# Optimization experiments

Measured on AMD Instinct MI355X. Metric: run time of the kernel, lower is better.

The kernel has to match this reference:

```python
import jax, jax.numpy as jnp
import numpy as np

ALPHA = 0.2  # LeakyReLU negative slope used by GAT attention


def _seg_softmax(scores, rows, n):
    # numerically stable softmax of per-edge scores grouped by destination row
    m = jax.ops.segment_max(scores, rows, num_segments=n)
    ex = jnp.exp(scores - m[rows])
    s = jax.ops.segment_sum(ex, rows, num_segments=n)
    return ex / s[rows]


def setup_inputs() -> dict:
    key = jax.random.key(0)
    ks = jax.random.split(key, 10)
    VOCAB, U, N, DEG = 200000, 50000, 20000, 16
    DIN, DOUT, H, ETYPES, EDIM = 64, 64, 4, 32, 64
    node_features = jax.random.normal(ks[0], (VOCAB, DIN), jnp.float32)
    W = jax.random.normal(ks[1], (H, DIN, DOUT), jnp.float32) * np.float32(np.sqrt(2.0 / (DIN + DOUT)))
    a_pos = jax.random.normal(ks[2], (H, 2 * DOUT), jnp.float32) * 0.1
    a_neg = jax.random.normal(ks[3], (H, 2 * DOUT), jnp.float32) * 0.1
    edge_embedding = jax.random.normal(ks[4], (ETYPES, EDIM), jnp.float32)
    edge_transform = jax.random.normal(ks[5], (EDIM, DOUT), jnp.float32) * np.float32(np.sqrt(2.0 / (EDIM + DOUT)))
    unique_nodes = jax.random.randint(ks[6], (U,), 0, VOCAB)
    row_unique = jax.random.randint(ks[7], (N,), 0, U)  # index of each output row's own node in the unique list
    # pos adjacency with self edges appended (adj_pos2 in the source)
    pos_row = jnp.concatenate([jnp.repeat(jnp.arange(N), DEG), jnp.arange(N)])
    pos_col = jnp.concatenate([jax.random.randint(ks[8], (N * DEG,), 0, U), row_unique])
    neg_row = jnp.repeat(jnp.arange(N), DEG)
    neg_col = jax.random.randint(ks[9], (N * DEG,), 0, U)
    return {
        "node_features": node_features, "W": W, "a_pos": a_pos, "a_neg": a_neg,
        "edge_embedding": edge_embedding, "edge_transform": edge_transform,
        "unique_nodes": unique_nodes, "row_unique": row_unique,
        "pos_row": pos_row, "pos_col": pos_col, "neg_row": neg_row, "neg_col": neg_col,
        "n_rows": N,
    }


def reference(node_features, W, a_pos, a_neg, edge_embedding, edge_transform,
              unique_nodes, row_unique, pos_row, pos_col, neg_row, neg_col, n_rows):
    embed = node_features[unique_nodes]                 # [U, Din] gather of unique node embeddings
    Wh = jnp.einsum('ud,hdo->huo', embed, W)            # [H, U, Dout]
    Dout = W.shape[-1]
    rows_all = jnp.concatenate([pos_row, neg_row])
    cols_all = jnp.concatenate([pos_col, neg_col])

    def head(Wh_h, ap, an):
        # per-node score halves (GAT trick: a^T[h_i || h_j] = a_dst.h_i + a_src.h_j)
        dst_p = (Wh_h @ ap[:Dout])[row_unique]          # [N]
        src_p = Wh_h @ ap[Dout:]                        # [U]
        dst_n = (Wh_h @ an[:Dout])[row_unique]
        src_n = Wh_h @ an[Dout:]
        e_pos = jax.nn.leaky_relu(dst_p[pos_row] + src_p[pos_col], ALPHA)
        e_neg = jax.nn.leaky_relu(dst_n[neg_row] + src_n[neg_col], ALPHA)
        att = _seg_softmax(jnp.concatenate([e_pos, e_neg]), rows_all, n_rows)  # joint softmax over pos+neg edges
        return jax.ops.segment_sum(att[:, None] * Wh_h[cols_all], rows_all, num_segments=n_rows)

    outs = jax.vmap(head)(Wh, a_pos, a_neg)             # [H, N, Dout]
    h_hidden = jax.nn.relu(jnp.transpose(outs, (1, 0, 2)).reshape(outs.shape[1], -1))  # concat heads -> ReLU
    edge_out = edge_embedding @ edge_transform          # edge-type projection
    return (h_hidden, edge_out)
```

## Files before the change

### kernel.cpp

```cpp
#include <hip/hip_runtime.h>
#include <hip/hip_bf16.h>
#include <hip/hip_fp16.h>
#include <math.h>

#define LRELU_ALPHA 0.2f

typedef __attribute__((ext_vector_type(8))) short bf16x8;
typedef __attribute__((ext_vector_type(4))) float f32x4;

__device__ __forceinline__ unsigned short f2bf(float f) {
    union { float f; unsigned u; } v; v.f = f;
    unsigned r = v.u + 0x7fffu + ((v.u >> 16) & 1u);
    return (unsigned short)(r >> 16);
}
__device__ __forceinline__ unsigned cvtpk(float lo, float hi) {
    unsigned r;
    asm("v_cvt_pk_bf16_f32 %0, %1, %2" : "=v"(r) : "v"(lo), "v"(hi));
    return r;
}
__device__ __forceinline__ __half2 u2h2(unsigned u) {
    union { unsigned u; __half2 h; } x; x.u = u; return x.h;
}
__device__ __forceinline__ unsigned h22u(__half2 h) {
    union { __half2 h; unsigned u; } x; x.h = h; return x.u;
}

__global__ void prep_kernel(const float* __restrict__ W,
                            const float* __restrict__ a_pos, const float* __restrict__ a_neg,
                            const float* __restrict__ ee, const float* __restrict__ et,
                            unsigned short* __restrict__ Wt, unsigned short* __restrict__ avB,
                            float* __restrict__ edge_out, int H, int ET) {
    const int HE = H * 4096, AV = H * 256;
    int t = blockIdx.x * blockDim.x + threadIdx.x;
    if (t < HE) {
        int k = t & 63, n = (t >> 6) & 63, h = t >> 12;
        Wt[((size_t)h * 64 + n) * 64 + k] = f2bf(W[(size_t)h * 4096 + k * 64 + n]);
    } else if (t < HE + AV) {
        int s = t - HE;
        int k = s & 63, q = (s >> 6) & 3, h = s >> 8;
        const float* a  = (q < 2 ? a_pos : a_neg) + (size_t)h * 128 + (q & 1) * 64;
        const float* wr = W + (size_t)h * 4096 + k * 64;
        float v = 0.f;
#pragma unroll
        for (int o = 0; o < 64; o += 4) {
            const float4 wv = *(const float4*)(wr + o);
            const float4 av = *(const float4*)(a + o);
            v = fmaf(wv.x, av.x, fmaf(wv.y, av.y, fmaf(wv.z, av.z, fmaf(wv.w, av.w, v))));
        }
        avB[((size_t)h * 4 + q) * 64 + k] = f2bf(v);
    } else {
        int s = t - HE - AV;
        if (s < ET * 64) {
            int e = s >> 6, o = s & 63;
            float acc = 0.f;
#pragma unroll
            for (int k = 0; k < 64; ++k)
                acc = fmaf(ee[e * 64 + k], et[k * 64 + o], acc);
            edge_out[s] = acc;
        }
    }
}

__global__ __launch_bounds__(256) void score_cvt_kernel(
    const float* __restrict__ nf, const unsigned short* __restrict__ avB,
    const int* __restrict__ un, unsigned short* __restrict__ embed16,
    float2* __restrict__ sc_dst, float2* __restrict__ sc_src, int U)
{
    const int wave = threadIdx.x >> 6;
    const int lane = threadIdx.x & 63;
    const int grp  = lane >> 4;
    const int r    = lane & 15;
    const long u0  = (long)blockIdx.x * 64 + wave * 16;
    if (u0 >= U) return;
    const long u  = u0 + r;
    const long ur = (u < U) ? u : (long)(U - 1);

    const float* erow = nf + (size_t)un[ur] * 64 + grp * 8;
    const float4 e0 = *(const float4*)(erow);
    const float4 e1 = *(const float4*)(erow + 4);
    const float4 e2 = *(const float4*)(erow + 32);
    const float4 e3 = *(const float4*)(erow + 36);

    union { unsigned d[4]; bf16x8 v; } A0, A1;
    A0.d[0] = cvtpk(e0.x, e0.y); A0.d[1] = cvtpk(e0.z, e0.w);
    A0.d[2] = cvtpk(e1.x, e1.y); A0.d[3] = cvtpk(e1.z, e1.w);
    A1.d[0] = cvtpk(e2.x, e2.y); A1.d[1] = cvtpk(e2.z, e2.w);
    A1.d[2] = cvtpk(e3.x, e3.y); A1.d[3] = cvtpk(e3.z, e3.w);

    if (u < U) {
        union { __half2 h2[4]; uint4 v; } F0, F1;
        F0.h2[0] = __floats2half2_rn(e0.x, e0.y); F0.h2[1] = __floats2half2_rn(e0.z, e0.w);
        F0.h2[2] = __floats2half2_rn(e1.x, e1.y); F0.h2[3] = __floats2half2_rn(e1.z, e1.w);
        F1.h2[0] = __floats2half2_rn(e2.x, e2.y); F1.h2[1] = __floats2half2_rn(e2.z, e2.w);
        F1.h2[2] = __floats2half2_rn(e3.x, e3.y); F1.h2[3] = __floats2half2_rn(e3.z, e3.w);
        *(uint4*)(embed16 + (size_t)u * 64 + grp * 8)      = F0.v;
        *(uint4*)(embed16 + (size_t)u * 64 + 32 + grp * 8) = F1.v;
    }

    f32x4 acc = (f32x4)(0.f);
    const unsigned short* wp = avB + (size_t)r * 64 + grp * 8;
    bf16x8 b0 = *(const bf16x8*)wp;
    bf16x8 b1 = *(const bf16x8*)(wp + 32);
    acc = __builtin_amdgcn_mfma_f32_16x16x32_bf16(b0, A0.v, acc, 0, 0, 0);
    acc = __builtin_amdgcn_mfma_f32_16x16x32_bf16(b1, A1.v, acc, 0, 0, 0);

    if (u < U) {
        sc_dst[(size_t)u * 4 + grp] = make_float2(acc[0], acc[2]);
        sc_src[(size_t)u * 4 + grp] = make_float2(acc[1], acc[3]);
    }
}

__global__ __launch_bounds__(256) void agg4_kernel(
    const int* __restrict__ pos_col, const int* __restrict__ neg_col,
    const unsigned short* __restrict__ embed16,
    const float2* __restrict__ sc_dst, const float2* __restrict__ sc_src,
    unsigned short* __restrict__ aggb, int N, int U)
{
    constexpr int DP = 16, NE = 33, NEP = 34;
    __shared__ int  s_col[4][NEP];
    __shared__ uint4 s_att[4][NEP];

    const int wave = threadIdx.x >> 6;
    const int lane = threadIdx.x & 63;
    const int i = blockIdx.x * 4 + wave;
    if (i >= N) return;

    int col = 0;
    if (lane < DP)       col = pos_col[(size_t)i * DP + lane];
    else if (lane == DP) col = pos_col[(size_t)N * DP + i];
    else if (lane < NE)  col = neg_col[(size_t)i * 16 + (lane - DP - 1)];

    const float4* ssv = (const float4*)sc_src;
    const float4 sA = ssv[2 * (size_t)(unsigned)col];
    const float4 sB = ssv[2 * (size_t)(unsigned)col + 1];
    const int u0s = __shfl(col, DP, 64);
    const float4* sdv = (const float4*)sc_dst;
    const float4 dA = sdv[2 * (size_t)(unsigned)u0s];
    const float4 dB = sdv[2 * (size_t)(unsigned)u0s + 1];

    const bool isp = (lane <= DP);
    float s0 = isp ? dA.x + sA.x : dA.y + sA.y;
    float s1 = isp ? dA.z + sA.z : dA.w + sA.w;
    float s2 = isp ? dB.x + sB.x : dB.y + sB.y;
    float s3 = isp ? dB.z + sB.z : dB.w + sB.w;
    s0 = (s0 > 0.f) ? s0 : LRELU_ALPHA * s0;
    s1 = (s1 > 0.f) ? s1 : LRELU_ALPHA * s1;
    s2 = (s2 > 0.f) ? s2 : LRELU_ALPHA * s2;
    s3 = (s3 > 0.f) ? s3 : LRELU_ALPHA * s3;
    if (lane >= NE) { s0 = s1 = s2 = s3 = -INFINITY; }

    float m0 = s0, m1 = s1, m2 = s2, m3 = s3;
#pragma unroll
    for (int off = 32; off; off >>= 1) {
        m0 = fmaxf(m0, __shfl_xor(m0, off, 64));
        m1 = fmaxf(m1, __shfl_xor(m1, off, 64));
        m2 = fmaxf(m2, __shfl_xor(m2, off, 64));
        m3 = fmaxf(m3, __shfl_xor(m3, off, 64));
    }
    const float x0 = (lane < NE) ? __expf(s0 - m0) : 0.f;
    const float x1 = (lane < NE) ? __expf(s1 - m1) : 0.f;
    const float x2 = (lane < NE) ? __expf(s2 - m2) : 0.f;
    const float x3 = (lane < NE) ? __expf(s3 - m3) : 0.f;
    float S0 = x0, S1 = x1, S2 = x2, S3 = x3;
#pragma unroll
    for (int off = 32; off; off >>= 1) {
        S0 += __shfl_xor(S0, off, 64);
        S1 += __shfl_xor(S1, off, 64);
        S2 += __shfl_xor(S2, off, 64);
        S3 += __shfl_xor(S3, off, 64);
    }
    const float a0f = __fdividef(x0, S0), a1f = __fdividef(x1, S1);
    const float a2f = __fdividef(x2, S2), a3f = __fdividef(x3, S3);

    if (lane < NEP) {
        uint4 a4;
        a4.x = h22u(__float2half2_rn(a0f));
        a4.y = h22u(__float2half2_rn(a1f));
        a4.z = h22u(__float2half2_rn(a2f));
        a4.w = h22u(__float2half2_rn(a3f));
        s_col[wave][lane] = col;
        s_att[wave][lane] = a4;
    }

    const int half = lane >> 5, mlo = lane & 31;
    const char* eb = (const char*)embed16 + (mlo << 2);
    __half2 ac0 = __float2half2_rn(0.f), ac1 = ac0, ac2 = ac0, ac3 = ac0;
#pragma unroll
    for (int t = 0; t < 17; ++t) {
        const int e = 2 * t + half;
        const int ce = s_col[wave][e];
        const uint4 a4 = s_att[wave][e];
        const unsigned v = *(const unsigned*)(eb + ((size_t)(unsigned)ce << 7));
        const __half2 vh = u2h2(v);
        ac0 = __hfma2(u2h2(a4.x), vh, ac0);
        ac1 = __hfma2(u2h2(a4.y), vh, ac1);
        ac2 = __hfma2(u2h2(a4.z), vh, ac2);
        ac3 = __hfma2(u2h2(a4.w), vh, ac3);
    }
    float2 f0 = __half22float2(ac0), f1 = __half22float2(ac1);
    float2 f2 = __half22float2(ac2), f3 = __half22float2(ac3);
    f0.x += __shfl_xor(f0.x, 32, 64); f0.y += __shfl_xor(f0.y, 32, 64);
    f1.x += __shfl_xor(f1.x, 32, 64); f1.y += __shfl_xor(f1.y, 32, 64);
    f2.x += __shfl_xor(f2.x, 32, 64); f2.y += __shfl_xor(f2.y, 32, 64);
    f3.x += __shfl_xor(f3.x, 32, 64); f3.y += __shfl_xor(f3.y, 32, 64);
    if (lane < 32) {
        unsigned* ap = (unsigned*)(aggb + (size_t)i * 256);
        ap[0 * 32 + mlo] = cvtpk(f0.x, f0.y);
        ap[1 * 32 + mlo] = cvtpk(f1.x, f1.y);
        ap[2 * 32 + mlo] = cvtpk(f2.x, f2.y);
        ap[3 * 32 + mlo] = cvtpk(f3.x, f3.y);
    }
}

__global__ __launch_bounds__(256) void out_gemm_kernel(
    const unsigned short* __restrict__ aggb, const unsigned short* __restrict__ Wt,
    float* __restrict__ out, int N, int H)
{
    const int wave = threadIdx.x >> 6;
    const int lane = threadIdx.x & 63;
    const int grp  = lane >> 4;
    const int r    = lane & 15;
    const long j = (long)blockIdx.x * 4 + wave;
    const int  h = (int)(j % H);
    const long i0 = (j / H) * 16;
    if (i0 >= N) return;
    const long i  = i0 + r;
    const long ir = (i < N) ? i : (long)(N - 1);

    const unsigned short* arow = aggb + ((size_t)ir * H + h) * 64 + grp * 8;
    bf16x8 a0 = *(const bf16x8*)arow;
    bf16x8 a1 = *(const bf16x8*)(arow + 32);

    f32x4 acc[4];
#pragma unroll
    for (int nt = 0; nt < 4; ++nt) {
        acc[nt] = (f32x4)(0.f);
        const unsigned short* wp = Wt + (((size_t)h * 64 + nt * 16 + r) * 64 + grp * 8);
        bf16x8 b0 = *(const bf16x8*)wp;
        bf16x8 b1 = *(const bf16x8*)(wp + 32);
        acc[nt] = __builtin_amdgcn_mfma_f32_16x16x32_bf16(b0, a0, acc[nt], 0, 0, 0);
        acc[nt] = __builtin_amdgcn_mfma_f32_16x16x32_bf16(b1, a1, acc[nt], 0, 0, 0);
    }
    if (i < N) {
        float* orow = out + ((size_t)i * H + h) * 64;
#pragma unroll
        for (int nt = 0; nt < 4; ++nt) {
            float4 o;
            o.x = fmaxf(acc[nt][0], 0.f); o.y = fmaxf(acc[nt][1], 0.f);
            o.z = fmaxf(acc[nt][2], 0.f); o.w = fmaxf(acc[nt][3], 0.f);
            *(float4*)(orow + nt * 16 + grp * 4) = o;
        }
    }
}

__global__ void embed_cvt_generic(const float* __restrict__ nf, const int* __restrict__ un,
                                  unsigned short* __restrict__ embed16, int U) {
    long t = (long)blockIdx.x * blockDim.x + threadIdx.x;
    if (t >= (long)U * 64) return;
    union { __half h; unsigned short s; } c;
    c.h = __float2half_rn(nf[(size_t)un[t >> 6] * 64 + (t & 63)]);
    embed16[t] = c.s;
}
__global__ void score_generic(const unsigned short* __restrict__ embed16,
                              const unsigned short* __restrict__ avB,
                              float2* __restrict__ sc_dst, float2* __restrict__ sc_src,
                              int U, int H) {
    long t = (long)blockIdx.x * blockDim.x + threadIdx.x;
    if (t >= (long)U * H) return;
    const long u = t / H; const int h = (int)(t % H);
    float s[4];
    for (int q = 0; q < 4; ++q) {
        float acc = 0.f;
        for (int k = 0; k < 64; ++k) {
            union { unsigned short s; __half h; } w; w.s = embed16[u * 64 + k];
            union { unsigned u; float f; } b; b.u = ((unsigned)avB[((size_t)h * 4 + q) * 64 + k]) << 16;
            acc = fmaf(__half2float(w.h), b.f, acc);
        }
        s[q] = acc;
    }
    sc_dst[u * H + h] = make_float2(s[0], s[2]);
    sc_src[u * H + h] = make_float2(s[1], s[3]);
}
__global__ __launch_bounds__(256) void agg_generic(
    const int* __restrict__ pos_col, const int* __restrict__ neg_col,
    const unsigned short* __restrict__ embed16,
    const float2* __restrict__ sc_dst, const float2* __restrict__ sc_src,
    unsigned short* __restrict__ aggb, int N, int U, int DEGP, int DEGN, int H)
{
    const int wave = threadIdx.x >> 6;
    const int lane = threadIdx.x & 63;
    const long j = (long)blockIdx.x * 4 + wave;
    const int i = (int)(j % N);
    const int h = (int)(j / N);
    if (h >= H) return;
    const int NE = DEGP + 1 + DEGN;

    int col = 0;
    if (lane < DEGP)       col = pos_col[(size_t)i * DEGP + lane];
    else if (lane == DEGP) col = pos_col[(size_t)N * DEGP + i];
    else if (lane < NE)    col = neg_col[(size_t)i * DEGN + (lane - DEGP - 1)];
    const float2 ss = sc_src[(size_t)col * H + h];
    const int u0s = __shfl(col, DEGP, 64);
    const float2 sd = sc_dst[(size_t)u0s * H + h];
    float score = -INFINITY;
    if (lane < NE) {
        const float raw = (lane <= DEGP) ? sd.x + ss.x : sd.y + ss.y;
        score = (raw > 0.f) ? raw : LRELU_ALPHA * raw;
    }
    float m = score;
#pragma unroll
    for (int off = 32; off; off >>= 1) m = fmaxf(m, __shfl_xor(m, off, 64));
    const float ex = (lane < NE) ? __expf(score - m) : 0.f;
    float S = ex;
#pragma unroll
    for (int off = 32; off; off >>= 1) S += __shfl_xor(S, off, 64);
    const float att = __fdividef(ex, S);

    float acc = 0.f;
    for (int e = 0; e < NE; ++e) {
        const int   ce = __shfl(col, e, 64);
        const float ae = __shfl(att, e, 64);
        union { unsigned short s; __half h; } w; w.s = embed16[(size_t)(unsigned)ce * 64 + lane];
        acc = fmaf(ae, __half2float(w.h), acc);
    }
    aggb[((size_t)i * H + h) * 64 + lane] = f2bf(acc);
}

extern "C" void kernel_launch(void* const* d_in, const int* in_sizes, int n_in,
                              void* d_out, int out_size, void* d_ws, size_t ws_size,
                              hipStream_t stream) {
    const float* nf     = (const float*)d_in[0];
    const float* W      = (const float*)d_in[1];
    const float* a_pos  = (const float*)d_in[2];
    const float* a_neg  = (const float*)d_in[3];
    const float* ee     = (const float*)d_in[4];
    const float* et     = (const float*)d_in[5];
    const int* unique_nodes = (const int*)d_in[6];
    const int* pos_col  = (const int*)d_in[9];
    const int* neg_col  = (const int*)d_in[11];

    const int U    = in_sizes[6];
    const int N    = in_sizes[7];
    const int Epos = in_sizes[8];
    const int Eneg = in_sizes[10];
    const int H    = in_sizes[1] / (64 * 64);
    const int DEGN = Eneg / N;
    const int DEGP = Epos / N - 1;
    const int ET   = in_sizes[4] / 64;

    char* ws = (char*)d_ws;
    auto alloc = [&](size_t bytes) { char* p = ws; ws += (bytes + 255) & ~(size_t)255; return p; };
    unsigned short* embed16 = (unsigned short*)alloc((size_t)U * 64 * 2);
    float2*         sc_dst  = (float2*)alloc((size_t)U * H * 8);
    float2*         sc_src  = (float2*)alloc((size_t)U * H * 8);
    unsigned short* aggb    = (unsigned short*)alloc((size_t)N * H * 64 * 2);
    unsigned short* Wt      = (unsigned short*)alloc((size_t)H * 4096 * 2);
    unsigned short* avB     = (unsigned short*)alloc((size_t)H * 256 * 2);
    float* out = (float*)d_out;

    const int PT = H * 4096 + H * 256 + ET * 64;
    prep_kernel<<<(PT + 255) / 256, 256, 0, stream>>>(W, a_pos, a_neg, ee, et, Wt, avB,
                                                      out + (size_t)N * H * 64, H, ET);

    if (H == 4 && DEGP == 16 && DEGN == 16) {
        score_cvt_kernel<<<(U + 63) / 64, 256, 0, stream>>>(nf, avB, unique_nodes,
                                                            embed16, sc_dst, sc_src, U);
        agg4_kernel<<<(N + 3) / 4, 256, 0, stream>>>(pos_col, neg_col, embed16,
                                                     sc_dst, sc_src, aggb, N, U);
    } else {
        embed_cvt_generic<<<(int)(((long)U * 64 + 255) / 256), 256, 0, stream>>>(
            nf, unique_nodes, embed16, U);
        score_generic<<<(int)(((long)U * H + 255) / 256), 256, 0, stream>>>(
            embed16, avB, sc_dst, sc_src, U, H);
        agg_generic<<<(int)(((long)N * H + 3) / 4), 256, 0, stream>>>(
            pos_col, neg_col, embed16, sc_dst, sc_src, aggb, N, U, DEGP, DEGN, H);
    }

    const long tiles = ((long)N + 15) / 16;
    out_gemm_kernel<<<(int)((tiles * H + 3) / 4), 256, 0, stream>>>(aggb, Wt, out, N, H);
}
```

Baseline: 49.48 us.

## Fuse attention aggregation with per-head output GEMM and drop softmax max pass

Merges the aggregation kernel and the output projection GEMM into one 512-thread kernel. Each wave aggregates two destination rows, the 16 rows per block are staged in LDS as fp16, and four waves then run fp16 MFMA against W to write the ReLU output directly. This removes the global round trip of the intermediate aggregate buffer and one kernel launch. It also switches W and the MFMA path from bf16 to fp16, and drops the max-subtraction reduction in the softmax, which risks exp overflow for large scores. A new N%16 requirement gates the fast path.

```diff
diff --git a/kernel.cpp b/kernel.cpp
--- a/kernel.cpp
+++ b/kernel.cpp
@@ -7,11 +7,15 @@
 
 typedef __attribute__((ext_vector_type(8))) short bf16x8;
 typedef __attribute__((ext_vector_type(4))) float f32x4;
+typedef _Float16 f16x8 __attribute__((ext_vector_type(8)));
 
 __device__ __forceinline__ unsigned short f2bf(float f) {
     union { float f; unsigned u; } v; v.f = f;
     unsigned r = v.u + 0x7fffu + ((v.u >> 16) & 1u);
     return (unsigned short)(r >> 16);
+}
+__device__ __forceinline__ unsigned short f2h(float f) {
+    union { __half h; unsigned short s; } c; c.h = __float2half_rn(f); return c.s;
 }
 __device__ __forceinline__ unsigned cvtpk(float lo, float hi) {
     unsigned r;
@@ -34,7 +38,7 @@
     int t = blockIdx.x * blockDim.x + threadIdx.x;
     if (t < HE) {
         int k = t & 63, n = (t >> 6) & 63, h = t >> 12;
-        Wt[((size_t)h * 64 + n) * 64 + k] = f2bf(W[(size_t)h * 4096 + k * 64 + n]);
+        Wt[((size_t)h * 64 + n) * 64 + k] = f2h(W[(size_t)h * 4096 + k * 64 + n]);
     } else if (t < HE + AV) {
         int s = t - HE;
         int k = s & 63, q = (s >> 6) & 3, h = s >> 8;
@@ -110,139 +114,169 @@
     }
 }
 
-__global__ __launch_bounds__(256) void agg4_kernel(
+__global__ __launch_bounds__(512) void aggemm_kernel(
     const int* __restrict__ pos_col, const int* __restrict__ neg_col,
     const unsigned short* __restrict__ embed16,
     const float2* __restrict__ sc_dst, const float2* __restrict__ sc_src,
-    unsigned short* __restrict__ aggb, int N, int U)
+    const unsigned short* __restrict__ Wt,
+    float* __restrict__ out, int N, int U)
 {
-    constexpr int DP = 16, NE = 33, NEP = 34;
-    __shared__ int  s_col[4][NEP];
-    __shared__ uint4 s_att[4][NEP];
+    constexpr int DP = 16, NE = 33, NEP = 36;
+    __shared__ int   s_col[8][2][NEP];
+    __shared__ uint4 s_att[8][2][NEP];
+    __shared__ __align__(16) unsigned short s_agg[16][256];
 
     const int wave = threadIdx.x >> 6;
     const int lane = threadIdx.x & 63;
-    const int i = blockIdx.x * 4 + wave;
-    if (i >= N) return;
-
-    int col = 0;
-    if (lane < DP)       col = pos_col[(size_t)i * DP + lane];
-    else if (lane == DP) col = pos_col[(size_t)N * DP + i];
-    else if (lane < NE)  col = neg_col[(size_t)i * 16 + (lane - DP - 1)];
+    const int iA = blockIdx.x * 16 + wave * 2;
+    const int iB = iA + 1;
+
+    int colA = 0, colB = 0;
+    if (lane < DP)       { colA = pos_col[(size_t)iA * DP + lane];
+                           colB = pos_col[(size_t)iB * DP + lane]; }
+    else if (lane == DP) { colA = pos_col[(size_t)N * DP + iA];
+                           colB = pos_col[(size_t)N * DP + iB]; }
+    else if (lane < NE)  { colA = neg_col[(size_t)iA * 16 + (lane - DP - 1)];
+                           colB = neg_col[(size_t)iB * 16 + (lane - DP - 1)]; }
 
     const float4* ssv = (const float4*)sc_src;
-    const float4 sA = ssv[2 * (size_t)(unsigned)col];
-    const float4 sB = ssv[2 * (size_t)(unsigned)col + 1];
-    const int u0s = __shfl(col, DP, 64);
+    const float4 sA0 = ssv[2 * (size_t)(unsigned)colA];
+    const float4 sA1 = ssv[2 * (size_t)(unsigned)colA + 1];
+    const float4 sB0 = ssv[2 * (size_t)(unsigned)colB];
+    const float4 sB1 = ssv[2 * (size_t)(unsigned)colB + 1];
+    const int uA = __shfl(colA, DP, 64), uB = __shfl(colB, DP, 64);
     const float4* sdv = (const float4*)sc_dst;
-    const float4 dA = sdv[2 * (size_t)(unsigned)u0s];
-    const float4 dB = sdv[2 * (size_t)(unsigned)u0s + 1];
+    const float4 dA0 = sdv[2 * (size_t)(unsigned)uA];
+    const float4 dA1 = sdv[2 * (size_t)(unsigned)uA + 1];
+    const float4 dB0 = sdv[2 * (size_t)(unsigned)uB];
+    const float4 dB1 = sdv[2 * (size_t)(unsigned)uB + 1];
 
     const bool isp = (lane <= DP);
-    float s0 = isp ? dA.x + sA.x : dA.y + sA.y;
-    float s1 = isp ? dA.z + sA.z : dA.w + sA.w;
-    float s2 = isp ? dB.x + sB.x : dB.y + sB.y;
-    float s3 = isp ? dB.z + sB.z : dB.w + sB.w;
-    s0 = (s0 > 0.f) ? s0 : LRELU_ALPHA * s0;
-    s1 = (s1 > 0.f) ? s1 : LRELU_ALPHA * s1;
-    s2 = (s2 > 0.f) ? s2 : LRELU_ALPHA * s2;
-    s3 = (s3 > 0.f) ? s3 : LRELU_ALPHA * s3;
-    if (lane >= NE) { s0 = s1 = s2 = s3 = -INFINITY; }
-
-    float m0 = s0, m1 = s1, m2 = s2, m3 = s3;
+    float a_s0 = isp ? dA0.x + sA0.x : dA0.y + sA0.y;
+    float a_s1 = isp ? dA0.z + sA0.z : dA0.w + sA0.w;
+    float a_s2 = isp ? dA1.x + sA1.x : dA1.y + sA1.y;
+    float a_s3 = isp ? dA1.z + sA1.z : dA1.w + sA1.w;
+    float b_s0 = isp ? dB0.x + sB0.x : dB0.y + sB0.y;
+    float b_s1 = isp ? dB0.z + sB0.z : dB0.w + sB0.w;
+    float b_s2 = isp ? dB1.x + sB1.x : dB1.y + sB1.y;
+    float b_s3 = isp ? dB1.z + sB1.z : dB1.w + sB1.w;
+    a_s0 = (a_s0 > 0.f) ? a_s0 : LRELU_ALPHA * a_s0;
+    a_s1 = (a_s1 > 0.f) ? a_s1 : LRELU_ALPHA * a_s1;
+    a_s2 = (a_s2 > 0.f) ? a_s2 : LRELU_ALPHA * a_s2;
+    a_s3 = (a_s3 > 0.f) ? a_s3 : LRELU_ALPHA * a_s3;
+    b_s0 = (b_s0 > 0.f) ? b_s0 : LRELU_ALPHA * b_s0;
+    b_s1 = (b_s1 > 0.f) ? b_s1 : LRELU_ALPHA * b_s1;
+    b_s2 = (b_s2 > 0.f) ? b_s2 : LRELU_ALPHA * b_s2;
+    b_s3 = (b_s3 > 0.f) ? b_s3 : LRELU_ALPHA * b_s3;
+
+    const bool act = (lane < NE);
+    float ax0 = act ? __expf(a_s0) : 0.f, ax1 = act ? __expf(a_s1) : 0.f;
+    float ax2 = act ? __expf(a_s2) : 0.f, ax3 = act ? __expf(a_s3) : 0.f;
+    float bx0 = act ? __expf(b_s0) : 0.f, bx1 = act ? __expf(b_s1) : 0.f;
+    float bx2 = act ? __expf(b_s2) : 0.f, bx3 = act ? __expf(b_s3) : 0.f;
+    float aS0 = ax0, aS1 = ax1, aS2 = ax2, aS3 = ax3;
+    float bS0 = bx0, bS1 = bx1, bS2 = bx2, bS3 = bx3;
 #pragma unroll
     for (int off = 32; off; off >>= 1) {
-        m0 = fmaxf(m0, __shfl_xor(m0, off, 64));
-        m1 = fmaxf(m1, __shfl_xor(m1, off, 64));
-        m2 = fmaxf(m2, __shfl_xor(m2, off, 64));
-        m3 = fmaxf(m3, __shfl_xor(m3, off, 64));
-    }
-    const float x0 = (lane < NE) ? __expf(s0 - m0) : 0.f;
-    const float x1 = (lane < NE) ? __expf(s1 - m1) : 0.f;
-    const float x2 = (lane < NE) ? __expf(s2 - m2) : 0.f;
-    const float x3 = (lane < NE) ? __expf(s3 - m3) : 0.f;
-    float S0 = x0, S1 = x1, S2 = x2, S3 = x3;
-#pragma unroll
-    for (int off = 32; off; off >>= 1) {
-        S0 += __shfl_xor(S0, off, 64);
-        S1 += __shfl_xor(S1, off, 64);
-        S2 += __shfl_xor(S2, off, 64);
-        S3 += __shfl_xor(S3, off, 64);
-    }
-    const float a0f = __fdividef(x0, S0), a1f = __fdividef(x1, S1);
-    const float a2f = __fdividef(x2, S2), a3f = __fdividef(x3, S3);
-
+        aS0 += __shfl_xor(aS0, off, 64); aS1 += __shfl_xor(aS1, off, 64);
+        aS2 += __shfl_xor(aS2, off, 64); aS3 += __shfl_xor(aS3, off, 64);
+        bS0 += __shfl_xor(bS0, off, 64); bS1 += __shfl_xor(bS1, off, 64);
+        bS2 += __shfl_xor(bS2, off, 64); bS3 += __shfl_xor(bS3, off, 64);
+    }
     if (lane < NEP) {
-        uint4 a4;
-        a4.x = h22u(__float2half2_rn(a0f));
-        a4.y = h22u(__float2half2_rn(a1f));
-        a4.z = h22u(__float2half2_rn(a2f));
-        a4.w = h22u(__float2half2_rn(a3f));
-        s_col[wave][lane] = col;
-        s_att[wave][lane] = a4;
-    }
-
-    const int half = lane >> 5, mlo = lane & 31;
-    const char* eb = (const char*)embed16 + (mlo << 2);
-    __half2 ac0 = __float2half2_rn(0.f), ac1 = ac0, ac2 = ac0, ac3 = ac0;
-#pragma unroll
-    for (int t = 0; t < 17; ++t) {
-        const int e = 2 * t + half;
-        const int ce = s_col[wave][e];
-        const uint4 a4 = s_att[wave][e];
-        const unsigned v = *(const unsigned*)(eb + ((size_t)(unsigned)ce << 7));
-        const __half2 vh = u2h2(v);
-        ac0 = __hfma2(u2h2(a4.x), vh, ac0);
-        ac1 = __hfma2(u2h2(a4.y), vh, ac1);
-        ac2 = __hfma2(u2h2(a4.z), vh, ac2);
-        ac3 = __hfma2(u2h2(a4.w), vh, ac3);
-    }
-    float2 f0 = __half22float2(ac0), f1 = __half22float2(ac1);
-    float2 f2 = __half22float2(ac2), f3 = __half22float2(ac3);
-    f0.x += __shfl_xor(f0.x, 32, 64); f0.y += __shfl_xor(f0.y, 32, 64);
-    f1.x += __shfl_xor(f1.x, 32, 64); f1.y += __shfl_xor(f1.y, 32, 64);
-    f2.x += __shfl_xor(f2.x, 32, 64); f2.y += __shfl_xor(f2.y, 32, 64);
-    f3.x += __shfl_xor(f3.x, 32, 64); f3.y += __shfl_xor(f3.y, 32, 64);
-    if (lane < 32) {
-        unsigned* ap = (unsigned*)(aggb + (size_t)i * 256);
-        ap[0 * 32 + mlo] = cvtpk(f0.x, f0.y);
-        ap[1 * 32 + mlo] = cvtpk(f1.x, f1.y);
-        ap[2 * 32 + mlo] = cvtpk(f2.x, f2.y);
-        ap[3 * 32 + mlo] = cvtpk(f3.x, f3.y);
-    }
-}
-
-__global__ __launch_bounds__(256) void out_gemm_kernel(
-    const unsigned short* __restrict__ aggb, const unsigned short* __restrict__ Wt,
-    float* __restrict__ out, int N, int H)
-{
-    const int wave = threadIdx.x >> 6;
-    const int lane = threadIdx.x & 63;
-    const int grp  = lane >> 4;
-    const int r    = lane & 15;
-    const long j = (long)blockIdx.x * 4 + wave;
-    const int  h = (int)(j % H);
-    const long i0 = (j / H) * 16;
-    if (i0 >= N) return;
-    const long i  = i0 + r;
-    const long ir = (i < N) ? i : (long)(N - 1);
-
-    const unsigned short* arow = aggb + ((size_t)ir * H + h) * 64 + grp * 8;
-    bf16x8 a0 = *(const bf16x8*)arow;
-    bf16x8 a1 = *(const bf16x8*)(arow + 32);
-
-    f32x4 acc[4];
-#pragma unroll
-    for (int nt = 0; nt < 4; ++nt) {
-        acc[nt] = (f32x4)(0.f);
-        const unsigned short* wp = Wt + (((size_t)h * 64 + nt * 16 + r) * 64 + grp * 8);
-        bf16x8 b0 = *(const bf16x8*)wp;
-        bf16x8 b1 = *(const bf16x8*)(wp + 32);
-        acc[nt] = __builtin_amdgcn_mfma_f32_16x16x32_bf16(b0, a0, acc[nt], 0, 0, 0);
-        acc[nt] = __builtin_amdgcn_mfma_f32_16x16x32_bf16(b1, a1, acc[nt], 0, 0, 0);
-    }
-    if (i < N) {
-        float* orow = out + ((size_t)i * H + h) * 64;
+        uint4 tA, tB;
+        tA.x = h22u(__float2half2_rn(__fdividef(ax0, aS0)));
+        tA.y = h22u(__float2half2_rn(__fdividef(ax1, aS1)));
+        tA.z = h22u(__float2half2_rn(__fdividef(ax2, aS2)));
+        tA.w = h22u(__float2half2_rn(__fdividef(ax3, aS3)));
+        tB.x = h22u(__float2half2_rn(__fdividef(bx0, bS0)));
+        tB.y = h22u(__float2half2_rn(__fdividef(bx1, bS1)));
+        tB.z = h22u(__float2half2_rn(__fdividef(bx2, bS2)));
+        tB.w = h22u(__float2half2_rn(__fdividef(bx3, bS3)));
+        s_col[wave][0][lane] = colA;  s_att[wave][0][lane] = tA;
+        s_col[wave][1][lane] = colB;  s_att[wave][1][lane] = tB;
+    }
+
+    const int sub = lane >> 4;
+    const int c   = lane & 15;
+    const char* eb = (const char*)embed16 + (c << 3);
+    __half2 accA[4][2], accB[4][2];
+#pragma unroll
+    for (int h = 0; h < 4; ++h)
+        for (int d = 0; d < 2; ++d) {
+            accA[h][d] = __float2half2_rn(0.f);
+            accB[h][d] = __float2half2_rn(0.f);
+        }
+#pragma unroll
+    for (int t = 0; t < 9; ++t) {
+        const int   e  = 4 * t + sub;
+        const int   cA = s_col[wave][0][e];
+        const int   cB = s_col[wave][1][e];
+        const uint2 vA = *(const uint2*)(eb + ((size_t)(unsigned)cA << 7));
+        const uint2 vB = *(const uint2*)(eb + ((size_t)(unsigned)cB << 7));
+        const uint4 tA = s_att[wave][0][e];
+        const uint4 tB = s_att[wave][1][e];
+        const __half2 vA0 = u2h2(vA.x), vA1 = u2h2(vA.y);
+        const __half2 vB0 = u2h2(vB.x), vB1 = u2h2(vB.y);
+        accA[0][0] = __hfma2(u2h2(tA.x), vA0, accA[0][0]);
+        accA[0][1] = __hfma2(u2h2(tA.x), vA1, accA[0][1]);
+        accA[1][0] = __hfma2(u2h2(tA.y), vA0, accA[1][0]);
+        accA[1][1] = __hfma2(u2h2(tA.y), vA1, accA[1][1]);
+        accA[2][0] = __hfma2(u2h2(tA.z), vA0, accA[2][0]);
+        accA[2][1] = __hfma2(u2h2(tA.z), vA1, accA[2][1]);
+        accA[3][0] = __hfma2(u2h2(tA.w), vA0, accA[3][0]);
+        accA[3][1] = __hfma2(u2h2(tA.w), vA1, accA[3][1]);
+        accB[0][0] = __hfma2(u2h2(tB.x), vB0, accB[0][0]);
+        accB[0][1] = __hfma2(u2h2(tB.x), vB1, accB[0][1]);
+        accB[1][0] = __hfma2(u2h2(tB.y), vB0, accB[1][0]);
+        accB[1][1] = __hfma2(u2h2(tB.y), vB1, accB[1][1]);
+        accB[2][0] = __hfma2(u2h2(tB.z), vB0, accB[2][0]);
+        accB[2][1] = __hfma2(u2h2(tB.z), vB1, accB[2][1]);
+        accB[3][0] = __hfma2(u2h2(tB.w), vB0, accB[3][0]);
+        accB[3][1] = __hfma2(u2h2(tB.w), vB1, accB[3][1]);
+    }
+#pragma unroll
+    for (int h = 0; h < 4; ++h)
+#pragma unroll
+        for (int d = 0; d < 2; ++d) {
+            unsigned ua = h22u(accA[h][d]);
+            ua = h22u(__hadd2(u2h2(ua), u2h2(__shfl_xor((int)ua, 16, 64))));
+            ua = h22u(__hadd2(u2h2(ua), u2h2(__shfl_xor((int)ua, 32, 64))));
+            accA[h][d] = u2h2(ua);
+            unsigned ub = h22u(accB[h][d]);
+            ub = h22u(__hadd2(u2h2(ub), u2h2(__shfl_xor((int)ub, 16, 64))));
+            ub = h22u(__hadd2(u2h2(ub), u2h2(__shfl_xor((int)ub, 32, 64))));
+            accB[h][d] = u2h2(ub);
+        }
+    if (sub == 0) {
+#pragma unroll
+        for (int h = 0; h < 4; ++h) {
+            uint2 wA, wB;
+            wA.x = h22u(accA[h][0]); wA.y = h22u(accA[h][1]);
+            wB.x = h22u(accB[h][0]); wB.y = h22u(accB[h][1]);
+            *(uint2*)((char*)&s_agg[wave * 2][h * 64] + c * 8)     = wA;
+            *(uint2*)((char*)&s_agg[wave * 2 + 1][h * 64] + c * 8) = wB;
+        }
+    }
+    __syncthreads();
+
+    if (wave < 4) {
+        const int h   = wave;
+        const int grp = lane >> 4;
+        const int r   = lane & 15;
+        const f16x8 a0 = *(const f16x8*)((const char*)&s_agg[r][h * 64] + grp * 16);
+        const f16x8 a1 = *(const f16x8*)((const char*)&s_agg[r][h * 64 + 32] + grp * 16);
+        f32x4 acc[4];
+#pragma unroll
+        for (int nt = 0; nt < 4; ++nt) {
+            acc[nt] = (f32x4)(0.f);
+            const unsigned short* wp = Wt + (((size_t)h * 64 + nt * 16 + r) * 64 + grp * 8);
+            const f16x8 b0 = *(const f16x8*)wp;
+            const f16x8 b1 = *(const f16x8*)(wp + 32);
+            acc[nt] = __builtin_amdgcn_mfma_f32_16x16x32_f16(b0, a0, acc[nt], 0, 0, 0);
+            acc[nt] = __builtin_amdgcn_mfma_f32_16x16x32_f16(b1, a1, acc[nt], 0, 0, 0);
+        }
+        float* orow = out + ((size_t)(blockIdx.x * 16 + r) * 4 + h) * 64;
 #pragma unroll
         for (int nt = 0; nt < 4; ++nt) {
             float4 o;
@@ -257,9 +291,7 @@
                                   unsigned short* __restrict__ embed16, int U) {
     long t = (long)blockIdx.x * blockDim.x + threadIdx.x;
     if (t >= (long)U * 64) return;
-    union { __half h; unsigned short s; } c;
-    c.h = __float2half_rn(nf[(size_t)un[t >> 6] * 64 + (t & 63)]);
-    embed16[t] = c.s;
+    embed16[t] = f2h(nf[(size_t)un[t >> 6] * 64 + (t & 63)]);
 }
 __global__ void score_generic(const unsigned short* __restrict__ embed16,
                               const unsigned short* __restrict__ avB,
@@ -323,7 +355,46 @@
         union { unsigned short s; __half h; } w; w.s = embed16[(size_t)(unsigned)ce * 64 + lane];
         acc = fmaf(ae, __half2float(w.h), acc);
     }
-    aggb[((size_t)i * H + h) * 64 + lane] = f2bf(acc);
+    aggb[((size_t)i * H + h) * 64 + lane] = f2h(acc);
+}
+__global__ __launch_bounds__(256) void out_gemm_generic(
+    const unsigned short* __restrict__ aggb, const unsigned short* __restrict__ Wt,
+    float* __restrict__ out, int N, int H)
+{
+    const int wave = threadIdx.x >> 6;
+    const int lane = threadIdx.x & 63;
+    const int grp  = lane >> 4;
+    const int r    = lane & 15;
+    const long j = (long)blockIdx.x * 4 + wave;
+    const int  h = (int)(j % H);
+    const long i0 = (j / H) * 16;
+    if (i0 >= N) return;
+    const long i  = i0 + r;
+    const long ir = (i < N) ? i : (long)(N - 1);
+
+    const unsigned short* arow = aggb + ((size_t)ir * H + h) * 64 + grp * 8;
+    const f16x8 a0 = *(const f16x8*)arow;
+    const f16x8 a1 = *(const f16x8*)(arow + 32);
+    f32x4 acc[4];
+#pragma unroll
+    for (int nt = 0; nt < 4; ++nt) {
+        acc[nt] = (f32x4)(0.f);
+        const unsigned short* wp = Wt + (((size_t)h * 64 + nt * 16 + r) * 64 + grp * 8);
+        const f16x8 b0 = *(const f16x8*)wp;
+        const f16x8 b1 = *(const f16x8*)(wp + 32);
+        acc[nt] = __builtin_amdgcn_mfma_f32_16x16x32_f16(b0, a0, acc[nt], 0, 0, 0);
+        acc[nt] = __builtin_amdgcn_mfma_f32_16x16x32_f16(b1, a1, acc[nt], 0, 0, 0);
+    }
+    if (i < N) {
+        float* orow = out + ((size_t)i * H + h) * 64;
+#pragma unroll
+        for (int nt = 0; nt < 4; ++nt) {
+            float4 o;
+            o.x = fmaxf(acc[nt][0], 0.f); o.y = fmaxf(acc[nt][1], 0.f);
+            o.z = fmaxf(acc[nt][2], 0.f); o.w = fmaxf(acc[nt][3], 0.f);
+            *(float4*)(orow + nt * 16 + grp * 4) = o;
+        }
+    }
 }
 
 extern "C" void kernel_launch(void* const* d_in, const int* in_sizes, int n_in,
@@ -362,11 +433,11 @@
     prep_kernel<<<(PT + 255) / 256, 256, 0, stream>>>(W, a_pos, a_neg, ee, et, Wt, avB,
                                                       out + (size_t)N * H * 64, H, ET);
 
-    if (H == 4 && DEGP == 16 && DEGN == 16) {
+    if (H == 4 && DEGP == 16 && DEGN == 16 && (N % 16) == 0) {
         score_cvt_kernel<<<(U + 63) / 64, 256, 0, stream>>>(nf, avB, unique_nodes,
                                                             embed16, sc_dst, sc_src, U);
-        agg4_kernel<<<(N + 3) / 4, 256, 0, stream>>>(pos_col, neg_col, embed16,
-                                                     sc_dst, sc_src, aggb, N, U);
+        aggemm_kernel<<<N / 16, 512, 0, stream>>>(pos_col, neg_col, embed16,
+                                                  sc_dst, sc_src, Wt, out, N, U);
     } else {
         embed_cvt_generic<<<(int)(((long)U * 64 + 255) / 256), 256, 0, stream>>>(
             nf, unique_nodes, embed16, U);
@@ -374,8 +445,7 @@
             embed16, avB, sc_dst, sc_src, U, H);
         agg_generic<<<(int)(((long)N * H + 3) / 4), 256, 0, stream>>>(
             pos_col, neg_col, embed16, sc_dst, sc_src, aggb, N, U, DEGP, DEGN, H);
-    }
-
-    const long tiles = ((long)N + 15) / 16;
-    out_gemm_kernel<<<(int)((tiles * H + 3) / 4), 256, 0, stream>>>(aggb, Wt, out, N, H);
-}
+        const long tiles = ((long)N + 15) / 16;
+        out_gemm_generic<<<(int)((tiles * H + 3) / 4), 256, 0, stream>>>(aggb, Wt, out, N, H);
+    }
+}
```

After: 47.57 us. 1.04x faster.
